# Performance work log

Measured on AMD Instinct MI355X. Metric: run time of the kernel, lower is better.

## Reference

```python
import jax, jax.numpy as jnp
import numpy as np

N_OSC = 128
N_AUDIO = 32768
NYQUIST = 22050 / 2.0
BASE_FREQ = 40.0 / NYQUIST
MAX_FREQ = 9000.0 / NYQUIST
FREQ_RANGE = MAX_FREQ - BASE_FREQ


def _interp_linear(a, out_size):
    # torch F.interpolate(mode='linear', align_corners=False) along last axis
    T = a.shape[-1]
    scale = T / out_size
    pos = (jnp.arange(out_size, dtype=a.dtype) + 0.5) * scale - 0.5
    pos = jnp.clip(pos, 0.0, T - 1)
    i0 = jnp.floor(pos).astype(jnp.int32)
    i1 = jnp.minimum(i0 + 1, T - 1)
    w = pos - i0.astype(a.dtype)
    return a[..., i0] * (1.0 - w) + a[..., i1] * w


def setup_inputs() -> dict:
    key = jax.random.key(0)
    k1, k2, k3, k4 = jax.random.split(key, 4)
    batch, channels, time = 4, 128, 128
    x = jax.random.normal(k1, (batch, channels, time), dtype=jnp.float32)
    # Conv1d(input_channels, n_osc*2, kernel=1) -> weight [2*n_osc, C], bias [2*n_osc]
    W = jax.random.normal(k2, (2 * N_OSC, channels), dtype=jnp.float32) * (1.0 / np.sqrt(channels))
    b = jax.random.normal(k3, (2 * N_OSC,), dtype=jnp.float32) * 0.01
    baselines = jax.random.uniform(k4, (N_OSC, 2), dtype=jnp.float32, minval=0.0, maxval=0.1)
    return {"x": x, "W": W, "b": b, "baselines": baselines}


def reference(x, W, b, baselines):
    batch, channels, time = x.shape
    # 1x1 conv = per-timestep matmul: [B, 2*n_osc, T]
    h = jnp.einsum('bct,oc->bot', x, W) + b[None, :, None]
    h = h.reshape(batch, N_OSC, 2, time)
    h = h * 0.01 + baselines[None, :, :, None]
    r = h[:, :, 0, :]
    i = h[:, :, 1, :]
    amp = jnp.sqrt(r * r + i * i)          # torch.norm over dim=2
    freq = jnp.arctan2(i, r) / np.pi       # torch.angle / pi
    freq = freq ** 2
    amp = amp ** 2
    amp = BASE_FREQ + amp * FREQ_RANGE
    amp = _interp_linear(amp, N_AUDIO)     # [B, n_osc, N_AUDIO]
    freq = _interp_linear(freq, N_AUDIO)
    phase = jnp.cumsum(freq * np.pi, axis=-1)
    osc = jnp.sin(phase) * amp
    osc = jnp.sum(osc, axis=1, keepdims=True)  # [B, 1, N_AUDIO]
    return osc
```

## Files before the change

### kernel.cpp

```cpp
#include <hip/hip_runtime.h>
#include <math.h>

#define BATCH 4
#define CH 128
#define NOSC 128
#define TK 128
#define NAUD 32768
#define NVS 129


__global__ __launch_bounds__(512) void osc1_kernel(
    const float* __restrict__ x, const float* __restrict__ W,
    const float* __restrict__ bvec, const float* __restrict__ baselines,
    float* __restrict__ seg)
{
    const int blk = blockIdx.x;
    const int b = blk >> 7, o = blk & 127;
    const int tid = threadIdx.x;
    const int k = tid & 127;
    const int c0 = __builtin_amdgcn_readfirstlane(tid >> 7) * 32;

    const float* __restrict__ Wr = W + (2*o)*CH;
    const float* __restrict__ Wi = Wr + CH;
    const float* xb = x + b*CH*TK + k;

    float re = 0.f, im = 0.f;
    {
        float xv[32];
        #pragma unroll
        for (int u = 0; u < 32; ++u) xv[u] = xb[(c0+u)*TK];
        #pragma unroll
        for (int u = 0; u < 32; ++u) { re = fmaf(xv[u], Wr[c0+u], re); im = fmaf(xv[u], Wi[c0+u], im); }
    }

    __shared__ float sRe[512], sIm[512];
    sRe[tid] = re; sIm[tid] = im;
    __syncthreads();

    __shared__ float fsh[TK], ash[TK];
    __shared__ double wtot;
    float fr = 0.f, amp = 0.f;
    if (tid < 128) {
        float rr = sRe[tid] + sRe[tid+128] + sRe[tid+256] + sRe[tid+384] + bvec[2*o];
        float ii = sIm[tid] + sIm[tid+128] + sIm[tid+256] + sIm[tid+384] + bvec[2*o+1];
        rr = fmaf(rr, 0.01f, baselines[2*o]);
        ii = fmaf(ii, 0.01f, baselines[2*o+1]);
        const float BASEF  = 40.0f/11025.0f;
        const float RANGEF = 8960.0f/11025.0f;
        amp = fmaf(fmaf(rr, rr, ii*ii), RANGEF, BASEF);
        float th = atan2f(ii, rr) * (1.0f/3.14159265358979323846f);
        fr = th*th;
        fsh[k] = fr; ash[k] = amp;
    }
    __syncthreads();

    double ev = 0.0;
    if (tid < 128) {
        ev = (k == 0) ? 128.0*(double)fr
                      : 128.0*((double)fsh[k-1] + (double)fr);
        const int lane = tid & 63;
        #pragma unroll
        for (int d = 1; d < 64; d <<= 1) {
            double up = __shfl_up(ev, d);
            if (lane >= d) ev += up;
        }
        if (tid == 63) wtot = ev;
    }
    __syncthreads();
    if (tid < 128) {
        if (tid >= 64) ev += wtot;
        double xrev = ev * 0.5;
        float cRev = (float)(xrev - floor(xrev));

        float* base = seg + ((size_t)(b*NVS)*NOSC + o)*8;
        const int vs = k + 1;
        float f0h = 0.5f*fr;
        float dfh = (k <= 126) ? 0.5f*(fsh[k+1] - fr) : 0.0f;
        float da  = (k <= 126) ? (ash[k+1] - amp) : 0.0f;
        float* p = base + (size_t)vs*NOSC*8;
        *(float4*)p = make_float4(f0h, dfh, cRev, amp);
        p[4] = da;
        if (k == 0) {
            *(float4*)base = make_float4(f0h, 0.0f, 0.0f, amp);
            base[4] = 0.0f;
        }
    }
}

__global__ __launch_bounds__(512) void osc2_kernel(
    const float* __restrict__ seg, float* __restrict__ out)
{
    const int blk = blockIdx.x;
    const int b   = blk >> 7;
    const int z   = blk & 127;
    const int tid = threadIdx.x;
    const int s   = tid & 255;
    const int g   = tid >> 8;

    __shared__ float4 tupA[256];
    __shared__ float4 tupB[256];
    __shared__ float  red[512];

    int t;
    float jp1;
    const float4* srcA = (const float4*)(seg + ((size_t)(b*NVS) + (z == 0 ? 0 : z))*NOSC*8);
    if (z == 0) {
        const float4* srcB = (const float4*)(seg + ((size_t)(b*NVS) + 128)*NOSC*8);
        if (tid < 256) tupA[tid]       = srcA[tid];
        else           tupB[tid - 256] = srcB[tid - 256];
        t   = (s < 128) ? s : (NAUD - 256 + s);
        jp1 = (float)((s & 127) + 1);
    } else {
        if (tid < 256) tupA[tid] = srcA[tid];
        t   = (2*z - 1)*128 + s;
        jp1 = (float)(s + 1);
    }
    __syncthreads();

    const float jsq = jp1*jp1*(1.0f/512.0f);
    const float w   = (2.0f*jp1 - 1.0f)*(1.0f/512.0f);

    const float* basep = (const float*)((z == 0 && s >= 128) ? &tupB[g*128] : &tupA[g*128]);
    float acc = 0.0f;
    #pragma unroll 8
    for (int i = 0; i < 64; ++i) {
        float4 v = *(const float4*)(basep + i*8);
        float da = basep[i*8 + 4];
        float rev = fmaf(v.y, jsq, fmaf(jp1, v.x, v.z));
        float fr_;
        asm("v_fract_f32 %0, %1" : "=v"(fr_) : "v"(rev));
        float sn;
        asm("v_sin_f32 %0, %1" : "=v"(sn) : "v"(fr_));
        acc = fmaf(fmaf(da, w, v.w), sn, acc);
    }

    red[tid] = acc;
    __syncthreads();
    if (tid < 256)
        out[b*NAUD + t] = red[tid] + red[tid + 256];
}

extern "C" void kernel_launch(void* const* d_in, const int* in_sizes, int n_in,
                              void* d_out, int out_size, void* d_ws, size_t ws_size,
                              hipStream_t stream)
{
    const float* x         = (const float*)d_in[0];
    const float* W         = (const float*)d_in[1];
    const float* bvec      = (const float*)d_in[2];
    const float* baselines = (const float*)d_in[3];
    float* out = (float*)d_out;
    float* seg = (float*)d_ws;

    osc1_kernel<<<BATCH*NOSC, 512, 0, stream>>>(x, W, bvec, baselines, seg);
    osc2_kernel<<<BATCH*128, 512, 0, stream>>>(seg, out);
}
```

Before: 15.55 us.

## Register-tile four samples per thread in osc2 to reuse LDS oscillator loads

Remaps osc2 so each thread computes four output samples over 16 oscillators instead of one sample over 64 oscillators, with eight oscillator groups reduced through a larger shared array. Each LDS read of oscillator parameters is reused across four samples, cutting shared-memory traffic per sine evaluation and adding independent accumulators for ILP. In exchange the final reduction grows from 2 to 8 partial sums per output, register use rises, and the z==0 block gets a separate path.

```diff
diff --git a/kernel.cpp b/kernel.cpp
--- a/kernel.cpp
+++ b/kernel.cpp
@@ -94,50 +94,107 @@
     const int b   = blk >> 7;
     const int z   = blk & 127;
     const int tid = threadIdx.x;
-    const int s   = tid & 255;
-    const int g   = tid >> 8;
+    const int s   = tid & 63;
+    const int g   = tid >> 6;
 
     __shared__ float4 tupA[256];
     __shared__ float4 tupB[256];
-    __shared__ float  red[512];
-
-    int t;
-    float jp1;
+    __shared__ float  red[8][256];
+
     const float4* srcA = (const float4*)(seg + ((size_t)(b*NVS) + (z == 0 ? 0 : z))*NOSC*8);
     if (z == 0) {
         const float4* srcB = (const float4*)(seg + ((size_t)(b*NVS) + 128)*NOSC*8);
         if (tid < 256) tupA[tid]       = srcA[tid];
         else           tupB[tid - 256] = srcB[tid - 256];
-        t   = (s < 128) ? s : (NAUD - 256 + s);
-        jp1 = (float)((s & 127) + 1);
     } else {
         if (tid < 256) tupA[tid] = srcA[tid];
-        t   = (2*z - 1)*128 + s;
-        jp1 = (float)(s + 1);
-    }
-    __syncthreads();
-
-    const float jsq = jp1*jp1*(1.0f/512.0f);
-    const float w   = (2.0f*jp1 - 1.0f)*(1.0f/512.0f);
-
-    const float* basep = (const float*)((z == 0 && s >= 128) ? &tupB[g*128] : &tupA[g*128]);
-    float acc = 0.0f;
-    #pragma unroll 8
-    for (int i = 0; i < 64; ++i) {
-        float4 v = *(const float4*)(basep + i*8);
-        float da = basep[i*8 + 4];
-        float rev = fmaf(v.y, jsq, fmaf(jp1, v.x, v.z));
-        float fr_;
-        asm("v_fract_f32 %0, %1" : "=v"(fr_) : "v"(rev));
-        float sn;
-        asm("v_sin_f32 %0, %1" : "=v"(sn) : "v"(fr_));
-        acc = fmaf(fmaf(da, w, v.w), sn, acc);
-    }
-
-    red[tid] = acc;
-    __syncthreads();
-    if (tid < 256)
-        out[b*NAUD + t] = red[tid] + red[tid + 256];
+    }
+    __syncthreads();
+
+    float acc0 = 0.f, acc1 = 0.f, acc2 = 0.f, acc3 = 0.f;
+    const float* bpA = (const float*)&tupA[g*32];
+    const float* bpB = (const float*)&tupB[g*32];
+
+    if (z != 0) {
+        float jp1_[4], jsq_[4], w_[4];
+        #pragma unroll
+        for (int m = 0; m < 4; ++m) {
+            float jp1 = (float)(64*m + s + 1);
+            jp1_[m] = jp1;
+            jsq_[m] = jp1*jp1*(1.0f/512.0f);
+            w_[m]   = (2.0f*jp1 - 1.0f)*(1.0f/512.0f);
+        }
+        #pragma unroll
+        for (int i = 0; i < 16; ++i) {
+            float4 v = *(const float4*)(bpA + i*8);
+            float da = bpA[i*8 + 4];
+            float fr_, sn;
+            float rev0 = fmaf(v.y, jsq_[0], fmaf(jp1_[0], v.x, v.z));
+            asm("v_fract_f32 %0, %1" : "=v"(fr_) : "v"(rev0));
+            asm("v_sin_f32 %0, %1"   : "=v"(sn)  : "v"(fr_));
+            acc0 = fmaf(fmaf(da, w_[0], v.w), sn, acc0);
+            float rev1 = fmaf(v.y, jsq_[1], fmaf(jp1_[1], v.x, v.z));
+            asm("v_fract_f32 %0, %1" : "=v"(fr_) : "v"(rev1));
+            asm("v_sin_f32 %0, %1"   : "=v"(sn)  : "v"(fr_));
+            acc1 = fmaf(fmaf(da, w_[1], v.w), sn, acc1);
+            float rev2 = fmaf(v.y, jsq_[2], fmaf(jp1_[2], v.x, v.z));
+            asm("v_fract_f32 %0, %1" : "=v"(fr_) : "v"(rev2));
+            asm("v_sin_f32 %0, %1"   : "=v"(sn)  : "v"(fr_));
+            acc2 = fmaf(fmaf(da, w_[2], v.w), sn, acc2);
+            float rev3 = fmaf(v.y, jsq_[3], fmaf(jp1_[3], v.x, v.z));
+            asm("v_fract_f32 %0, %1" : "=v"(fr_) : "v"(rev3));
+            asm("v_sin_f32 %0, %1"   : "=v"(sn)  : "v"(fr_));
+            acc3 = fmaf(fmaf(da, w_[3], v.w), sn, acc3);
+        }
+    } else {
+        float jp1_[2], jsq_[2], w_[2];
+        #pragma unroll
+        for (int m = 0; m < 2; ++m) {
+            float jp1 = (float)(64*m + s + 1);
+            jp1_[m] = jp1;
+            jsq_[m] = jp1*jp1*(1.0f/512.0f);
+            w_[m]   = (2.0f*jp1 - 1.0f)*(1.0f/512.0f);
+        }
+        #pragma unroll
+        for (int i = 0; i < 16; ++i) {
+            float4 vA = *(const float4*)(bpA + i*8);
+            float daA = bpA[i*8 + 4];
+            float4 vB = *(const float4*)(bpB + i*8);
+            float daB = bpB[i*8 + 4];
+            float fr_, sn;
+            float rev0 = fmaf(vA.y, jsq_[0], fmaf(jp1_[0], vA.x, vA.z));
+            asm("v_fract_f32 %0, %1" : "=v"(fr_) : "v"(rev0));
+            asm("v_sin_f32 %0, %1"   : "=v"(sn)  : "v"(fr_));
+            acc0 = fmaf(fmaf(daA, w_[0], vA.w), sn, acc0);
+            float rev1 = fmaf(vA.y, jsq_[1], fmaf(jp1_[1], vA.x, vA.z));
+            asm("v_fract_f32 %0, %1" : "=v"(fr_) : "v"(rev1));
+            asm("v_sin_f32 %0, %1"   : "=v"(sn)  : "v"(fr_));
+            acc1 = fmaf(fmaf(daA, w_[1], vA.w), sn, acc1);
+            float rev2 = fmaf(vB.y, jsq_[0], fmaf(jp1_[0], vB.x, vB.z));
+            asm("v_fract_f32 %0, %1" : "=v"(fr_) : "v"(rev2));
+            asm("v_sin_f32 %0, %1"   : "=v"(sn)  : "v"(fr_));
+            acc2 = fmaf(fmaf(daB, w_[0], vB.w), sn, acc2);
+            float rev3 = fmaf(vB.y, jsq_[1], fmaf(jp1_[1], vB.x, vB.z));
+            asm("v_fract_f32 %0, %1" : "=v"(fr_) : "v"(rev3));
+            asm("v_sin_f32 %0, %1"   : "=v"(sn)  : "v"(fr_));
+            acc3 = fmaf(fmaf(daB, w_[1], vB.w), sn, acc3);
+        }
+    }
+
+    red[g][      s] = acc0;
+    red[g][ 64 + s] = acc1;
+    red[g][128 + s] = acc2;
+    red[g][192 + s] = acc3;
+    __syncthreads();
+
+    if (tid < 256) {
+        float v = 0.f;
+        #pragma unroll
+        for (int gg = 0; gg < 8; ++gg) v += red[gg][tid];
+        int t = (z != 0) ? ((2*z - 1)*128 + tid)
+                         : ((tid < 128) ? tid : (NAUD - 256 + tid));
+        out[b*NAUD + t] = v;
+    }
 }
 
 extern "C" void kernel_launch(void* const* d_in, const int* in_sizes, int n_in,
```

New measurement: 15.07 us, median of 2. 1.03x faster.
